# Kernel optimization log

Hardware: AMD Instinct MI355X
Metric: run time of the kernel (lower is better)

The kernel has to match this reference:

```python
import jax, jax.numpy as jnp
import numpy as np

N_SRC = 200000   # source (input) nodes
N_DST = 50000    # destination (output) nodes; dst node i == src node i (block convention)
E = 800000       # edges
IN = 256
OUT = 64
H = 3
SLOPE = 0.2      # leaky_relu negative_slope


def setup_inputs() -> dict:
    key = jax.random.key(0)
    k0, k1, k2, k3, k4, k5 = jax.random.split(key, 6)
    x = jax.random.normal(k0, (N_SRC, IN), dtype=jnp.float32)
    W = jax.random.normal(k1, (H * OUT, IN), dtype=jnp.float32) * (1.0 / np.sqrt(IN))
    attn_l = jax.random.normal(k2, (1, H, OUT), dtype=jnp.float32) * 0.1
    attn_r = jax.random.normal(k3, (1, H, OUT), dtype=jnp.float32) * 0.1
    src = jax.random.randint(k4, (E,), 0, N_SRC, dtype=jnp.int32)
    dst = jnp.sort(jax.random.randint(k5, (E,), 0, N_DST, dtype=jnp.int32))
    return {"x": x, "W": W, "attn_l": attn_l, "attn_r": attn_r, "src": src, "dst": dst}


def reference(x, W, attn_l, attn_r, src, dst):
    # fc + reshape to heads: [N_src, H, F]
    feat = (x @ W.T).reshape(N_SRC, H, OUT)
    # per-head attention logits
    el = jnp.sum(feat * attn_l, axis=-1)          # [N_src, H]
    er = jnp.sum(feat[:N_DST] * attn_r, axis=-1)  # [N_dst, H] (self_gather of out nodes)
    # edge scores: apply_edge + leaky_relu -> [E, H]
    e = jax.nn.leaky_relu(el[src] + er[dst], negative_slope=SLOPE)
    # segmented max over incoming edges of each dst node (gather_local_max)
    m = jax.ops.segment_max(e, dst, num_segments=N_DST)
    m = jnp.where(jnp.isfinite(m), m, jnp.float32(0))  # empty segments -> 0
    m = jax.lax.stop_gradient(m)
    ex = jnp.exp(e - m[dst])                       # [E, H]
    s = jax.ops.segment_sum(ex, dst, num_segments=N_DST)  # [N_dst, H]
    s = jnp.where(s == 0, jnp.float32(1), s)       # sum_exponent[sum==0] = 1
    att = ex / s[dst]                              # [E, H]
    # attention_gather: sum over edges of att * src feature -> [N_dst, H, F]
    out = jax.ops.segment_sum(att[:, :, None] * feat[src], dst, num_segments=N_DST)
    return out.reshape(N_DST, H * OUT)
```

## Files before the change

kernel.cpp:

```cpp
#include <hip/hip_runtime.h>
#include <hip/hip_bf16.h>

#define N_SRCN 200000
#define N_DSTN 50000
#define NEDGE 800000
#define KIN 256
#define NF 192
#define SLOPE 0.2f
#define TILES16 12500
#define NWAVES 2048

typedef __attribute__((ext_vector_type(8))) short bf16x8;
typedef __attribute__((ext_vector_type(4))) float f32x4;

__device__ __forceinline__ unsigned short f2bf(float f) {
    union { float f; unsigned int u; } v; v.f = f;
    unsigned int u = v.u;
    return (unsigned short)((u + 0x7FFFu + ((u >> 16) & 1u)) >> 16);
}
__device__ __forceinline__ float bf2f(unsigned short h) {
    union { unsigned int u; float f; } v; v.u = ((unsigned int)h) << 16;
    return v.f;
}
__device__ __forceinline__ unsigned int cvt2(float lo, float hi) {
    __hip_bfloat162 h = __float22bfloat162_rn(float2{lo, hi});
    union { __hip_bfloat162 h; unsigned int u; } c; c.h = h;
    return c.u;
}
__device__ __forceinline__ void gl_lds16(const void* g, void* l) {
    __builtin_amdgcn_global_load_lds(
        (const __attribute__((address_space(1))) unsigned int*)g,
        (__attribute__((address_space(3))) unsigned int*)l, 16, 0, 0);
}

__global__ void prep_kernel(const float* __restrict__ W, unsigned short* __restrict__ Wp,
                            const int* __restrict__ dst, int* __restrict__ rp) {
    const int bid = blockIdx.x;
    if (bid < 24) {
        int tid = bid * 256 + threadIdx.x;
        if (tid >= 12 * 8 * 64) return;
        int lane = tid & 63;
        int g = tid >> 6;
        int nt = g % 12, ks = g / 12;
        int col = nt * 16 + (lane & 15);
        int k = ks * 32 + (lane >> 4) * 8;
        const float* wsrc = &W[col * KIN + k];
        unsigned short* o = &Wp[tid * 8];
        #pragma unroll
        for (int j = 0; j < 8; ++j) o[j] = f2bf(wsrc[j]);
    } else {
        int d = (bid - 24) * 256 + threadIdx.x;
        if (d > N_DSTN) return;
        int lo = 0, hi = NEDGE;
        while (lo < hi) {
            int mid = (lo + hi) >> 1;
            if (dst[mid] < d) lo = mid + 1; else hi = mid;
        }
        rp[d] = lo;
    }
}

__global__ void __launch_bounds__(512, 1)
gemm_feat(const float* __restrict__ x, const unsigned short* __restrict__ Wp,
          const float* __restrict__ attn_l, const float* __restrict__ attn_r,
          unsigned short* __restrict__ feat,
          float* __restrict__ el4, float* __restrict__ er4) {
    __shared__ unsigned short Bl[12 * 8 * 512];
    const int t = threadIdx.x;
    const int wid = t >> 6, lane = t & 63;
    const int al = lane & 15, ah = lane >> 4;

    #pragma unroll
    for (int i = 0; i < 12; ++i) {
        const int off = (i * 8 + wid) * 1024;
        gl_lds16((const char*)Wp + off + lane * 16, (char*)Bl + off);
    }
    asm volatile("s_waitcnt vmcnt(0)" ::: "memory");
    __syncthreads();

    float Al[12], Ar[12];
    #pragma unroll
    for (int nt = 0; nt < 12; ++nt) {
        Al[nt] = attn_l[nt * 16 + al];
        Ar[nt] = attn_r[nt * 16 + al];
    }

    const int gw = blockIdx.x * 8 + wid;
    for (int tile = gw; tile < TILES16; tile += NWAVES) {
        const int r0 = tile * 16;
        const float* xrow = &x[(size_t)(r0 + al) * KIN + ah * 8];

        f32x4 acc[12] = {};
        #pragma unroll
        for (int ks = 0; ks < 8; ++ks) {
            const float4 a0 = *(const float4*)&xrow[ks * 32];
            const float4 a1 = *(const float4*)&xrow[ks * 32 + 4];
            union { bf16x8 v; unsigned int u[4]; } av;
            av.u[0] = cvt2(a0.x, a0.y);
            av.u[1] = cvt2(a0.z, a0.w);
            av.u[2] = cvt2(a1.x, a1.y);
            av.u[3] = cvt2(a1.z, a1.w);
            #pragma unroll
            for (int nt = 0; nt < 12; ++nt) {
                const bf16x8 bv = *(const bf16x8*)&Bl[(ks * 12 + nt) * 512 + lane * 8];
                acc[nt] = __builtin_amdgcn_mfma_f32_16x16x32_bf16(av.v, bv, acc[nt], 0, 0, 0);
            }
        }

        #pragma unroll
        for (int nt = 0; nt < 12; ++nt) {
            const int col = nt * 16 + al;
            #pragma unroll
            for (int e = 0; e < 4; ++e) {
                const int row = r0 + ah * 4 + e;
                feat[(size_t)row * NF + col] = f2bf(acc[nt][e]);
            }
        }

        #pragma unroll
        for (int h = 0; h < 3; ++h) {
            #pragma unroll
            for (int e = 0; e < 4; ++e) {
                float sl = 0.f, sr = 0.f;
                #pragma unroll
                for (int q = 0; q < 4; ++q) {
                    const int nt = h * 4 + q;
                    sl += acc[nt][e] * Al[nt];
                    sr += acc[nt][e] * Ar[nt];
                }
                #pragma unroll
                for (int m = 1; m <= 8; m <<= 1) {
                    sl += __shfl_xor(sl, m);
                    sr += __shfl_xor(sr, m);
                }
                if (al == 0) {
                    const int row = r0 + ah * 4 + e;
                    el4[(size_t)row * 4 + h] = sl;
                    if (row < N_DSTN) er4[(size_t)row * 4 + h] = sr;
                }
            }
        }
    }
}

__launch_bounds__(256)
__global__ void gather_kernel(const unsigned short* __restrict__ feat,
                              const float* __restrict__ el4, const float* __restrict__ er4,
                              const int* __restrict__ src, const int* __restrict__ rp,
                              float* __restrict__ out) {
    const int lane = threadIdx.x & 63;
    const int d = (blockIdx.x * blockDim.x + threadIdx.x) >> 6;
    if (d >= N_DSTN) return;
    const int lo = rp[d], hi = rp[d + 1];
    const float4 erv = *(const float4*)&er4[(size_t)d * 4];

    float a0 = 0.f, a1 = 0.f, a2 = 0.f, s0 = 0.f, s1 = 0.f, s2 = 0.f;
    for (int base = lo; base < hi; base += 64) {
        const int cnt = min(64, hi - base);
        int sv = 0; float w0 = 0.f, w1 = 0.f, w2 = 0.f;
        if (lane < cnt) {
            sv = src[base + lane];
            const float4 elv = *(const float4*)&el4[(size_t)sv * 4];
            float e0 = elv.x + erv.x; e0 = e0 >= 0.f ? e0 : SLOPE * e0; w0 = __expf(e0);
            float e1 = elv.y + erv.y; e1 = e1 >= 0.f ? e1 : SLOPE * e1; w1 = __expf(e1);
            float e2 = elv.z + erv.z; e2 = e2 >= 0.f ? e2 : SLOPE * e2; w2 = __expf(e2);
        }
        int j = 0;
        for (; j + 8 <= cnt; j += 8) {
            unsigned short f0[8], f1[8], f2[8];
            float u0[8], u1[8], u2[8];
            #pragma unroll
            for (int q = 0; q < 8; ++q) {
                const int sj = __shfl(sv, j + q);
                const unsigned short* fp = &feat[(size_t)sj * NF + lane];
                f0[q] = fp[0]; f1[q] = fp[64]; f2[q] = fp[128];
                u0[q] = __shfl(w0, j + q);
                u1[q] = __shfl(w1, j + q);
                u2[q] = __shfl(w2, j + q);
            }
            #pragma unroll
            for (int q = 0; q < 8; ++q) {
                s0 += u0[q]; a0 += u0[q] * bf2f(f0[q]);
                s1 += u1[q]; a1 += u1[q] * bf2f(f1[q]);
                s2 += u2[q]; a2 += u2[q] * bf2f(f2[q]);
            }
        }
        for (; j < cnt; ++j) {
            const int sj = __shfl(sv, j);
            const float u0 = __shfl(w0, j);
            const float u1 = __shfl(w1, j);
            const float u2 = __shfl(w2, j);
            const unsigned short* fp = &feat[(size_t)sj * NF + lane];
            s0 += u0; a0 += u0 * bf2f(fp[0]);
            s1 += u1; a1 += u1 * bf2f(fp[64]);
            s2 += u2; a2 += u2 * bf2f(fp[128]);
        }
    }
    if (hi == lo) { s0 = 1.f; s1 = 1.f; s2 = 1.f; }
    float* op = &out[(size_t)d * NF];
    op[lane]       = a0 / s0;
    op[64 + lane]  = a1 / s1;
    op[128 + lane] = a2 / s2;
}

extern "C" void kernel_launch(void* const* d_in, const int* in_sizes, int n_in,
                              void* d_out, int out_size, void* d_ws, size_t ws_size,
                              hipStream_t stream) {
    const float* x      = (const float*)d_in[0];
    const float* W      = (const float*)d_in[1];
    const float* attn_l = (const float*)d_in[2];
    const float* attn_r = (const float*)d_in[3];
    const int*   src    = (const int*)d_in[4];
    const int*   dst    = (const int*)d_in[5];
    float* out = (float*)d_out;

    char* ws = (char*)d_ws;
    unsigned short* feat = (unsigned short*)ws;
    float* el4 = (float*)(ws + 76800000);
    float* er4 = (float*)(ws + 80000000);
    unsigned short* Wp = (unsigned short*)(ws + 80800000);
    int*   rp = (int*)(ws + 80898304);

    prep_kernel<<<24 + 196, 256, 0, stream>>>(W, Wp, dst, rp);
    gemm_feat<<<256, 512, 0, stream>>>(x, Wp, attn_l, attn_r, feat, el4, er4);
    gather_kernel<<<12500, 256, 0, stream>>>(feat, el4, er4, src, rp, out);
}
```

Measured before the change: 149.8 us.

## Fold attention projections into GEMM as extra column tile and prefetch next A tile

Precomputes W^T·attn_l and W^T·attn_r per head in the prep kernel and appends them as a 13th 16-column B tile, so the GEMM's MFMAs produce el/er directly. This replaces the per-tile epilogue dot products and cross-lane shuffles. It also software-pipelines the x loads by prefetching the next tile's fp32 rows into registers while the current tile computes. In exchange it adds one more MFMA column tile per k-step, and el/er now come from bf16-rounded projection weights, which changes numerics slightly.

```diff
diff --git a/kernel.cpp b/kernel.cpp
--- a/kernel.cpp
+++ b/kernel.cpp
@@ -9,6 +9,7 @@
 #define SLOPE 0.2f
 #define TILES16 12500
 #define NWAVES 2048
+#define NNT 13
 
 typedef __attribute__((ext_vector_type(8))) short bf16x8;
 typedef __attribute__((ext_vector_type(4))) float f32x4;
@@ -33,23 +34,40 @@
         (__attribute__((address_space(3))) unsigned int*)l, 16, 0, 0);
 }
 
-__global__ void prep_kernel(const float* __restrict__ W, unsigned short* __restrict__ Wp,
+__global__ void prep_kernel(const float* __restrict__ W,
+                            const float* __restrict__ attn_l, const float* __restrict__ attn_r,
+                            unsigned short* __restrict__ Wp,
                             const int* __restrict__ dst, int* __restrict__ rp) {
     const int bid = blockIdx.x;
-    if (bid < 24) {
+    if (bid < 26) {
         int tid = bid * 256 + threadIdx.x;
-        if (tid >= 12 * 8 * 64) return;
+        if (tid >= NNT * 8 * 64) return;
         int lane = tid & 63;
         int g = tid >> 6;
-        int nt = g % 12, ks = g / 12;
-        int col = nt * 16 + (lane & 15);
+        int nt = g % NNT, ks = g / NNT;
         int k = ks * 32 + (lane >> 4) * 8;
-        const float* wsrc = &W[col * KIN + k];
         unsigned short* o = &Wp[tid * 8];
-        #pragma unroll
-        for (int j = 0; j < 8; ++j) o[j] = f2bf(wsrc[j]);
+        if (nt < 12) {
+            int col = nt * 16 + (lane & 15);
+            const float* wsrc = &W[col * KIN + k];
+            #pragma unroll
+            for (int j = 0; j < 8; ++j) o[j] = f2bf(wsrc[j]);
+        } else {
+            int cc = lane & 15;
+            #pragma unroll
+            for (int j = 0; j < 8; ++j) {
+                float s = 0.f;
+                if (cc < 6) {
+                    const int h = cc < 3 ? cc : cc - 3;
+                    const float* aw = cc < 3 ? attn_l : attn_r;
+                    for (int f = 0; f < 64; ++f)
+                        s += aw[h * 64 + f] * W[(h * 64 + f) * KIN + k + j];
+                }
+                o[j] = f2bf(s);
+            }
+        }
     } else {
-        int d = (bid - 24) * 256 + threadIdx.x;
+        int d = (bid - 26) * 256 + threadIdx.x;
         if (d > N_DSTN) return;
         int lo = 0, hi = NEDGE;
         while (lo < hi) {
@@ -62,51 +80,63 @@
 
 __global__ void __launch_bounds__(512, 1)
 gemm_feat(const float* __restrict__ x, const unsigned short* __restrict__ Wp,
-          const float* __restrict__ attn_l, const float* __restrict__ attn_r,
           unsigned short* __restrict__ feat,
           float* __restrict__ el4, float* __restrict__ er4) {
-    __shared__ unsigned short Bl[12 * 8 * 512];
+    __shared__ unsigned short Bl[NNT * 8 * 512];
     const int t = threadIdx.x;
     const int wid = t >> 6, lane = t & 63;
     const int al = lane & 15, ah = lane >> 4;
 
     #pragma unroll
-    for (int i = 0; i < 12; ++i) {
+    for (int i = 0; i < 13; ++i) {
         const int off = (i * 8 + wid) * 1024;
         gl_lds16((const char*)Wp + off + lane * 16, (char*)Bl + off);
     }
     asm volatile("s_waitcnt vmcnt(0)" ::: "memory");
     __syncthreads();
 
-    float Al[12], Ar[12];
-    #pragma unroll
-    for (int nt = 0; nt < 12; ++nt) {
-        Al[nt] = attn_l[nt * 16 + al];
-        Ar[nt] = attn_r[nt * 16 + al];
-    }
-
     const int gw = blockIdx.x * 8 + wid;
+
+    #define LOADA(tl)                                                          \
+        {                                                                      \
+            const float* xrow = &x[(size_t)((tl) * 16 + al) * KIN + ah * 8];   \
+            _Pragma("unroll")                                                  \
+            for (int k = 0; k < 8; ++k) {                                      \
+                pf[2 * k]     = *(const float4*)&xrow[k * 32];                 \
+                pf[2 * k + 1] = *(const float4*)&xrow[k * 32 + 4];             \
+            }                                                                  \
+        }
+
+    float4 pf[16];
+    if (gw < TILES16) LOADA(gw)
+
     for (int tile = gw; tile < TILES16; tile += NWAVES) {
+        bf16x8 av[8];
+        #pragma unroll
+        for (int ks = 0; ks < 8; ++ks) {
+            union { bf16x8 v; unsigned int u[4]; } c;
+            c.u[0] = cvt2(pf[2 * ks].x,     pf[2 * ks].y);
+            c.u[1] = cvt2(pf[2 * ks].z,     pf[2 * ks].w);
+            c.u[2] = cvt2(pf[2 * ks + 1].x, pf[2 * ks + 1].y);
+            c.u[3] = cvt2(pf[2 * ks + 1].z, pf[2 * ks + 1].w);
+            av[ks] = c.v;
+        }
+        __builtin_amdgcn_sched_barrier(0);
+        const int nxt = tile + NWAVES;
+        if (nxt < TILES16) LOADA(nxt)
+        __builtin_amdgcn_sched_barrier(0);
+
+        f32x4 acc[NNT] = {};
+        #pragma unroll
+        for (int ks = 0; ks < 8; ++ks) {
+            #pragma unroll
+            for (int nt = 0; nt < NNT; ++nt) {
+                const bf16x8 bv = *(const bf16x8*)&Bl[(ks * NNT + nt) * 512 + lane * 8];
+                acc[nt] = __builtin_amdgcn_mfma_f32_16x16x32_bf16(av[ks], bv, acc[nt], 0, 0, 0);
+            }
+        }
+
         const int r0 = tile * 16;
-        const float* xrow = &x[(size_t)(r0 + al) * KIN + ah * 8];
-
-        f32x4 acc[12] = {};
-        #pragma unroll
-        for (int ks = 0; ks < 8; ++ks) {
-            const float4 a0 = *(const float4*)&xrow[ks * 32];
-            const float4 a1 = *(const float4*)&xrow[ks * 32 + 4];
-            union { bf16x8 v; unsigned int u[4]; } av;
-            av.u[0] = cvt2(a0.x, a0.y);
-            av.u[1] = cvt2(a0.z, a0.w);
-            av.u[2] = cvt2(a1.x, a1.y);
-            av.u[3] = cvt2(a1.z, a1.w);
-            #pragma unroll
-            for (int nt = 0; nt < 12; ++nt) {
-                const bf16x8 bv = *(const bf16x8*)&Bl[(ks * 12 + nt) * 512 + lane * 8];
-                acc[nt] = __builtin_amdgcn_mfma_f32_16x16x32_bf16(av.v, bv, acc[nt], 0, 0, 0);
-            }
-        }
-
         #pragma unroll
         for (int nt = 0; nt < 12; ++nt) {
             const int col = nt * 16 + al;
@@ -116,31 +146,15 @@
                 feat[(size_t)row * NF + col] = f2bf(acc[nt][e]);
             }
         }
-
-        #pragma unroll
-        for (int h = 0; h < 3; ++h) {
-            #pragma unroll
-            for (int e = 0; e < 4; ++e) {
-                float sl = 0.f, sr = 0.f;
-                #pragma unroll
-                for (int q = 0; q < 4; ++q) {
-                    const int nt = h * 4 + q;
-                    sl += acc[nt][e] * Al[nt];
-                    sr += acc[nt][e] * Ar[nt];
-                }
-                #pragma unroll
-                for (int m = 1; m <= 8; m <<= 1) {
-                    sl += __shfl_xor(sl, m);
-                    sr += __shfl_xor(sr, m);
-                }
-                if (al == 0) {
-                    const int row = r0 + ah * 4 + e;
-                    el4[(size_t)row * 4 + h] = sl;
-                    if (row < N_DSTN) er4[(size_t)row * 4 + h] = sr;
-                }
-            }
-        }
-    }
+        #pragma unroll
+        for (int e = 0; e < 4; ++e) {
+            const int row = r0 + ah * 4 + e;
+            const float v = acc[12][e];
+            if (al < 3) el4[(size_t)row * 4 + al] = v;
+            else if (al < 6 && row < N_DSTN) er4[(size_t)row * 4 + (al - 3)] = v;
+        }
+    }
+    #undef LOADA
 }
 
 __launch_bounds__(256)
@@ -219,9 +233,9 @@
     float* el4 = (float*)(ws + 76800000);
     float* er4 = (float*)(ws + 80000000);
     unsigned short* Wp = (unsigned short*)(ws + 80800000);
-    int*   rp = (int*)(ws + 80898304);
-
-    prep_kernel<<<24 + 196, 256, 0, stream>>>(W, Wp, dst, rp);
-    gemm_feat<<<256, 512, 0, stream>>>(x, Wp, attn_l, attn_r, feat, el4, er4);
+    int*   rp = (int*)(ws + 80906496);
+
+    prep_kernel<<<26 + 196, 256, 0, stream>>>(W, attn_l, attn_r, Wp, dst, rp);
+    gemm_feat<<<256, 512, 0, stream>>>(x, Wp, feat, el4, er4);
     gather_kernel<<<12500, 256, 0, stream>>>(feat, el4, er4, src, rp, out);
 }
```

After: 154.4 us. 3.1% more time.

## Split GEMM by head across blocks and store attention logits per head

Applied to the files above, without the earlier changes.

The feature GEMM now launches one block per (16-row-tile group, head): each block loads only that head's 64 weight columns into LDS, does one tile per wave with 4 accumulators, and writes el/er into separate per-head arrays instead of float4-strided arrays. Smaller LDS and register use allow up to 4 blocks per CU and many more waves to hide latency, replacing the previous persistent 256-block grid. The cost is that each x row is read three times, once per head block, which triples GEMM input traffic (partly served from cache). The gather kernel now does three scalar loads per edge from separate arrays instead of one float4 load.

```diff
diff --git a/kernel.cpp b/kernel.cpp
--- a/kernel.cpp
+++ b/kernel.cpp
@@ -8,7 +8,7 @@
 #define NF 192
 #define SLOPE 0.2f
 #define TILES16 12500
-#define NWAVES 2048
+#define NGRP 1563
 
 typedef __attribute__((ext_vector_type(8))) short bf16x8;
 typedef __attribute__((ext_vector_type(4))) float f32x4;
@@ -33,19 +33,21 @@
         (__attribute__((address_space(3))) unsigned int*)l, 16, 0, 0);
 }
 
-__global__ void prep_kernel(const float* __restrict__ W, unsigned short* __restrict__ Wp,
+__global__ void prep_kernel(const float* __restrict__ W, unsigned short* __restrict__ Wp3,
                             const int* __restrict__ dst, int* __restrict__ rp) {
     const int bid = blockIdx.x;
     if (bid < 24) {
         int tid = bid * 256 + threadIdx.x;
-        if (tid >= 12 * 8 * 64) return;
+        if (tid >= 96 * 64) return;
         int lane = tid & 63;
         int g = tid >> 6;
-        int nt = g % 12, ks = g / 12;
+        int h = g / 32, rem = g % 32;
+        int ks = rem / 4, q = rem % 4;
+        int nt = h * 4 + q;
         int col = nt * 16 + (lane & 15);
         int k = ks * 32 + (lane >> 4) * 8;
         const float* wsrc = &W[col * KIN + k];
-        unsigned short* o = &Wp[tid * 8];
+        unsigned short* o = &Wp3[(size_t)g * 512 + lane * 8];
         #pragma unroll
         for (int j = 0; j < 8; ++j) o[j] = f2bf(wsrc[j]);
     } else {
@@ -60,99 +62,103 @@
     }
 }
 
-__global__ void __launch_bounds__(512, 1)
-gemm_feat(const float* __restrict__ x, const unsigned short* __restrict__ Wp,
+__global__ void __launch_bounds__(512, 4)
+gemm_feat(const float* __restrict__ x, const unsigned short* __restrict__ Wp3,
           const float* __restrict__ attn_l, const float* __restrict__ attn_r,
           unsigned short* __restrict__ feat,
-          float* __restrict__ el4, float* __restrict__ er4) {
-    __shared__ unsigned short Bl[12 * 8 * 512];
+          float* __restrict__ el0, float* __restrict__ el1, float* __restrict__ el2,
+          float* __restrict__ er0, float* __restrict__ er1, float* __restrict__ er2) {
+    __shared__ unsigned short Bl[32 * 512];
     const int t = threadIdx.x;
     const int wid = t >> 6, lane = t & 63;
     const int al = lane & 15, ah = lane >> 4;
-
-    #pragma unroll
-    for (int i = 0; i < 12; ++i) {
+    const int grp = blockIdx.x / 3;
+    const int htype = blockIdx.x % 3;
+
+    const char* wsrc = (const char*)Wp3 + (size_t)htype * 32768;
+    #pragma unroll
+    for (int i = 0; i < 4; ++i) {
         const int off = (i * 8 + wid) * 1024;
-        gl_lds16((const char*)Wp + off + lane * 16, (char*)Bl + off);
+        gl_lds16(wsrc + off + lane * 16, (char*)Bl + off);
     }
     asm volatile("s_waitcnt vmcnt(0)" ::: "memory");
     __syncthreads();
 
-    float Al[12], Ar[12];
-    #pragma unroll
-    for (int nt = 0; nt < 12; ++nt) {
-        Al[nt] = attn_l[nt * 16 + al];
-        Ar[nt] = attn_r[nt * 16 + al];
-    }
-
-    const int gw = blockIdx.x * 8 + wid;
-    for (int tile = gw; tile < TILES16; tile += NWAVES) {
-        const int r0 = tile * 16;
-        const float* xrow = &x[(size_t)(r0 + al) * KIN + ah * 8];
-
-        f32x4 acc[12] = {};
-        #pragma unroll
-        for (int ks = 0; ks < 8; ++ks) {
-            const float4 a0 = *(const float4*)&xrow[ks * 32];
-            const float4 a1 = *(const float4*)&xrow[ks * 32 + 4];
-            union { bf16x8 v; unsigned int u[4]; } av;
-            av.u[0] = cvt2(a0.x, a0.y);
-            av.u[1] = cvt2(a0.z, a0.w);
-            av.u[2] = cvt2(a1.x, a1.y);
-            av.u[3] = cvt2(a1.z, a1.w);
-            #pragma unroll
-            for (int nt = 0; nt < 12; ++nt) {
-                const bf16x8 bv = *(const bf16x8*)&Bl[(ks * 12 + nt) * 512 + lane * 8];
-                acc[nt] = __builtin_amdgcn_mfma_f32_16x16x32_bf16(av.v, bv, acc[nt], 0, 0, 0);
-            }
-        }
-
-        #pragma unroll
-        for (int nt = 0; nt < 12; ++nt) {
-            const int col = nt * 16 + al;
-            #pragma unroll
-            for (int e = 0; e < 4; ++e) {
-                const int row = r0 + ah * 4 + e;
-                feat[(size_t)row * NF + col] = f2bf(acc[nt][e]);
-            }
-        }
-
-        #pragma unroll
-        for (int h = 0; h < 3; ++h) {
-            #pragma unroll
-            for (int e = 0; e < 4; ++e) {
-                float sl = 0.f, sr = 0.f;
-                #pragma unroll
-                for (int q = 0; q < 4; ++q) {
-                    const int nt = h * 4 + q;
-                    sl += acc[nt][e] * Al[nt];
-                    sr += acc[nt][e] * Ar[nt];
-                }
-                #pragma unroll
-                for (int m = 1; m <= 8; m <<= 1) {
-                    sl += __shfl_xor(sl, m);
-                    sr += __shfl_xor(sr, m);
-                }
-                if (al == 0) {
-                    const int row = r0 + ah * 4 + e;
-                    el4[(size_t)row * 4 + h] = sl;
-                    if (row < N_DSTN) er4[(size_t)row * 4 + h] = sr;
-                }
-            }
+    float Al[4], Ar[4];
+    #pragma unroll
+    for (int q = 0; q < 4; ++q) {
+        Al[q] = attn_l[(htype * 4 + q) * 16 + al];
+        Ar[q] = attn_r[(htype * 4 + q) * 16 + al];
+    }
+
+    const int tile = grp * 8 + wid;
+    if (tile >= TILES16) return;
+    const int r0 = tile * 16;
+    const float* xrow = &x[(size_t)(r0 + al) * KIN + ah * 8];
+
+    f32x4 acc[4] = {};
+    #pragma unroll
+    for (int ks = 0; ks < 8; ++ks) {
+        const float4 a0 = *(const float4*)&xrow[ks * 32];
+        const float4 a1 = *(const float4*)&xrow[ks * 32 + 4];
+        union { bf16x8 v; unsigned int u[4]; } av;
+        av.u[0] = cvt2(a0.x, a0.y);
+        av.u[1] = cvt2(a0.z, a0.w);
+        av.u[2] = cvt2(a1.x, a1.y);
+        av.u[3] = cvt2(a1.z, a1.w);
+        #pragma unroll
+        for (int q = 0; q < 4; ++q) {
+            const bf16x8 bv = *(const bf16x8*)&Bl[(ks * 4 + q) * 512 + lane * 8];
+            acc[q] = __builtin_amdgcn_mfma_f32_16x16x32_bf16(av.v, bv, acc[q], 0, 0, 0);
+        }
+    }
+
+    #pragma unroll
+    for (int q = 0; q < 4; ++q) {
+        const int col = (htype * 4 + q) * 16 + al;
+        #pragma unroll
+        for (int e = 0; e < 4; ++e) {
+            const int row = r0 + ah * 4 + e;
+            feat[(size_t)row * NF + col] = f2bf(acc[q][e]);
+        }
+    }
+
+    float* elh = htype == 0 ? el0 : (htype == 1 ? el1 : el2);
+    float* erh = htype == 0 ? er0 : (htype == 1 ? er1 : er2);
+    #pragma unroll
+    for (int e = 0; e < 4; ++e) {
+        float sl = 0.f, sr = 0.f;
+        #pragma unroll
+        for (int q = 0; q < 4; ++q) {
+            sl += acc[q][e] * Al[q];
+            sr += acc[q][e] * Ar[q];
+        }
+        #pragma unroll
+        for (int m = 1; m <= 8; m <<= 1) {
+            sl += __shfl_xor(sl, m);
+            sr += __shfl_xor(sr, m);
+        }
+        if (al == 0) {
+            const int row = r0 + ah * 4 + e;
+            elh[row] = sl;
+            if (row < N_DSTN) erh[row] = sr;
         }
     }
 }
 
 __launch_bounds__(256)
 __global__ void gather_kernel(const unsigned short* __restrict__ feat,
-                              const float* __restrict__ el4, const float* __restrict__ er4,
+                              const float* __restrict__ el0, const float* __restrict__ el1,
+                              const float* __restrict__ el2,
+                              const float* __restrict__ er0, const float* __restrict__ er1,
+                              const float* __restrict__ er2,
                               const int* __restrict__ src, const int* __restrict__ rp,
                               float* __restrict__ out) {
     const int lane = threadIdx.x & 63;
     const int d = (blockIdx.x * blockDim.x + threadIdx.x) >> 6;
     if (d >= N_DSTN) return;
     const int lo = rp[d], hi = rp[d + 1];
-    const float4 erv = *(const float4*)&er4[(size_t)d * 4];
+    const float erv0 = er0[d], erv1 = er1[d], erv2 = er2[d];
 
     float a0 = 0.f, a1 = 0.f, a2 = 0.f, s0 = 0.f, s1 = 0.f, s2 = 0.f;
     for (int base = lo; base < hi; base += 64) {
@@ -160,10 +166,9 @@
         int sv = 0; float w0 = 0.f, w1 = 0.f, w2 = 0.f;
         if (lane < cnt) {
             sv = src[base + lane];
-            const float4 elv = *(const float4*)&el4[(size_t)sv * 4];
-            float e0 = elv.x + erv.x; e0 = e0 >= 0.f ? e0 : SLOPE * e0; w0 = __expf(e0);
-            float e1 = elv.y + erv.y; e1 = e1 >= 0.f ? e1 : SLOPE * e1; w1 = __expf(e1);
-            float e2 = elv.z + erv.z; e2 = e2 >= 0.f ? e2 : SLOPE * e2; w2 = __expf(e2);
+            float e0 = el0[sv] + erv0; e0 = e0 >= 0.f ? e0 : SLOPE * e0; w0 = __expf(e0);
+            float e1 = el1[sv] + erv1; e1 = e1 >= 0.f ? e1 : SLOPE * e1; w1 = __expf(e1);
+            float e2 = el2[sv] + erv2; e2 = e2 >= 0.f ? e2 : SLOPE * e2; w2 = __expf(e2);
         }
         int j = 0;
         for (; j + 8 <= cnt; j += 8) {
@@ -216,12 +221,18 @@
 
     char* ws = (char*)d_ws;
     unsigned short* feat = (unsigned short*)ws;
-    float* el4 = (float*)(ws + 76800000);
-    float* er4 = (float*)(ws + 80000000);
-    unsigned short* Wp = (unsigned short*)(ws + 80800000);
-    int*   rp = (int*)(ws + 80898304);
-
-    prep_kernel<<<24 + 196, 256, 0, stream>>>(W, Wp, dst, rp);
-    gemm_feat<<<256, 512, 0, stream>>>(x, Wp, attn_l, attn_r, feat, el4, er4);
-    gather_kernel<<<12500, 256, 0, stream>>>(feat, el4, er4, src, rp, out);
-}
+    float* el0 = (float*)(ws + 76800000);
+    float* el1 = (float*)(ws + 77600000);
+    float* el2 = (float*)(ws + 78400000);
+    float* er0 = (float*)(ws + 79200000);
+    float* er1 = (float*)(ws + 79400000);
+    float* er2 = (float*)(ws + 79600000);
+    unsigned short* Wp3 = (unsigned short*)(ws + 79800000);
+    int*   rp = (int*)(ws + 79898304);
+
+    prep_kernel<<<24 + 196, 256, 0, stream>>>(W, Wp3, dst, rp);
+    gemm_feat<<<3 * NGRP, 512, 0, stream>>>(x, Wp3, attn_l, attn_r, feat,
+                                            el0, el1, el2, er0, er1, er2);
+    gather_kernel<<<12500, 256, 0, stream>>>(feat, el0, el1, el2, er0, er1, er2,
+                                             src, rp, out);
+}
```

Measured after the change: 191.7 us. 1.28x slower.
